# Kernel tuning notes

Hardware: AMD Instinct MI355X
Metric: run time of the kernel (lower is better)

## Reference

```python
import jax, jax.numpy as jnp
import numpy as np
from jax import lax

PRE_NMS_TOPN = 6000
POST_NMS_TOPN = 300
NMS_IOU = 0.7
VARIANCES = np.array([0.1, 0.1, 0.2, 0.2], dtype=np.float32)


def setup_inputs() -> dict:
    key = jax.random.key(0)
    k1, k2, k3, k4 = jax.random.split(key, 4)
    B, FH, FW, K = 32, 128, 128, 9
    A = FH * FW * K  # 147456 total anchors
    rpn_bbox_deltas = jax.random.normal(k1, (B, A, 4), dtype=jnp.float32) * 0.1
    rpn_labels = jax.random.normal(k2, (B, FH, FW, K), dtype=jnp.float32)
    # Anchors in [y1, x1, y2, x2] with y1<y2, x1<x2 on a ~1024px image.
    ctr = jax.random.uniform(k3, (A, 2), dtype=jnp.float32) * 1024.0
    wh = jax.random.uniform(k4, (A, 2), dtype=jnp.float32) * 224.0 + 32.0
    anchors = jnp.concatenate([ctr - 0.5 * wh, ctr + 0.5 * wh], axis=-1)
    return {"rpn_bbox_deltas": rpn_bbox_deltas, "rpn_labels": rpn_labels, "anchors": anchors}


def get_bboxes_from_deltas(anchors, deltas):
    # anchors: [A, 4] (y1,x1,y2,x2); deltas: [B, A, 4] (dy,dx,dh,dw)
    anc_w = anchors[..., 3] - anchors[..., 1]
    anc_h = anchors[..., 2] - anchors[..., 0]
    anc_cx = anchors[..., 1] + 0.5 * anc_w
    anc_cy = anchors[..., 0] + 0.5 * anc_h
    bb_w = jnp.exp(deltas[..., 3]) * anc_w
    bb_h = jnp.exp(deltas[..., 2]) * anc_h
    bb_cx = deltas[..., 1] * anc_w + anc_cx
    bb_cy = deltas[..., 0] * anc_h + anc_cy
    y1 = bb_cy - 0.5 * bb_h
    x1 = bb_cx - 0.5 * bb_w
    y2 = bb_h + y1
    x2 = bb_w + x1
    return jnp.stack([y1, x1, y2, x2], axis=-1)


def nms_per_image(boxes, scores, iou_threshold, num_keep):
    # boxes: [N, 4] sorted by descending score; scores: [N]
    y1, x1, y2, x2 = boxes[:, 0], boxes[:, 1], boxes[:, 2], boxes[:, 3]
    areas = (y2 - y1) * (x2 - x1)

    def step(scores_rem, _):
        idx = jnp.argmax(scores_rem)
        valid = jnp.isfinite(scores_rem[idx])
        b = boxes[idx]
        iy1 = jnp.maximum(b[0], y1)
        ix1 = jnp.maximum(b[1], x1)
        iy2 = jnp.minimum(b[2], y2)
        ix2 = jnp.minimum(b[3], x2)
        inter = jnp.clip(iy2 - iy1, 0.0) * jnp.clip(ix2 - ix1, 0.0)
        b_area = (b[2] - b[0]) * (b[3] - b[1])
        iou = inter / (areas + b_area - inter + 1e-9)
        # IoU(box, itself) == 1 > threshold, so the picked box is also suppressed.
        new_scores = jnp.where(iou > iou_threshold, -jnp.inf, scores_rem)
        return new_scores, (idx, valid)

    _, (keep_idx, valid) = lax.scan(step, scores, None, length=num_keep)
    vf = valid.astype(boxes.dtype)
    keep_boxes = boxes[keep_idx] * vf[:, None]  # zero-pad invalid slots
    keep_scores = scores[keep_idx] * vf
    return keep_boxes, keep_scores


def reference(rpn_bbox_deltas, rpn_labels, anchors):
    A = anchors.shape[0]
    B = rpn_bbox_deltas.shape[0]
    deltas = rpn_bbox_deltas.reshape(B, A, 4) * jnp.asarray(VARIANCES)
    labels = jax.nn.softmax(rpn_labels, axis=-1).reshape(B, A)
    rpn_bboxes = get_bboxes_from_deltas(anchors, deltas)  # [B, A, 4]
    # top-k pre-NMS filter (lax.top_k output is already sorted descending)
    pre_scores, pre_idx = lax.top_k(labels, PRE_NMS_TOPN)  # [B, P]
    pre_boxes = jnp.take_along_axis(rpn_bboxes, pre_idx[..., None], axis=1)  # [B, P, 4]
    nms_fn = lambda b, s: nms_per_image(b, s, NMS_IOU, POST_NMS_TOPN)
    roi_bboxes, roi_scores = jax.vmap(nms_fn)(pre_boxes, pre_scores)
    return roi_bboxes, roi_scores
```

## Files before the change

### kernel.cpp

```cpp
#include <hip/hip_runtime.h>
#include <cstdint>
#include <cstddef>

#pragma clang fp contract(off)

#define KCLS 9
#define PRE_N 6000
#define POST_N 300
#define NMS_IOU_T 0.7f
#define HIST_BLOCK 256
#define CHUNKS_PER_IMG 32
#define NMS_BLOCK 512
#define PICK_BLOCK 256
#define NSEG 8
#define SEG_CAP 2048
#define RANK_LDS 8192

#define SUPP(pb, pa, mbx, mar, out) \
    bool out; { \
        float iy1_ = fmaxf((pb).x, (mbx).x); \
        float ix1_ = fmaxf((pb).y, (mbx).y); \
        float iy2_ = fminf((pb).z, (mbx).z); \
        float ix2_ = fminf((pb).w, (mbx).w); \
        float ih_ = iy2_ - iy1_; ih_ = ih_ > 0.f ? ih_ : 0.f; \
        float iw_ = ix2_ - ix1_; iw_ = iw_ > 0.f ? iw_ : 0.f; \
        float inter_ = ih_ * iw_; \
        float den_ = (mar) + (pa) - inter_ + 1e-9f; \
        float hi_ = 0.7000007f * den_; \
        float lo_ = 0.6999993f * den_; \
        out = inter_ > hi_; \
        if (inter_ >= lo_ && inter_ <= hi_) out = (inter_ / den_) > NMS_IOU_T; \
    }

__global__ void __launch_bounds__(256)
softmax_hist_kernel(const float* __restrict__ labels,
                    float* __restrict__ scores,
                    unsigned int* __restrict__ ghist,
                    int gpi) {
    __shared__ float buf[256 * KCLS];
    __shared__ unsigned int h[2048];
    const int tid = threadIdx.x;
    for (int i = tid; i < 2048; i += 256) h[i] = 0u;

    const size_t gbase = (size_t)blockIdx.x * (256 * KCLS);
    const float4* lin4 = (const float4*)(labels + gbase);
    float4* b4 = (float4*)buf;
    for (int i = tid; i < 576; i += 256) b4[i] = lin4[i];
    __syncthreads();

    float v[KCLS];
    float m = -1e30f;
    #pragma unroll
    for (int k = 0; k < KCLS; ++k) { v[k] = buf[tid * KCLS + k]; m = fmaxf(m, v[k]); }
    float e[KCLS];
    float s = 0.f;
    #pragma unroll
    for (int k = 0; k < KCLS; ++k) { e[k] = expf(v[k] - m); s += e[k]; }
    #pragma unroll
    for (int k = 0; k < KCLS; ++k) {
        float r = e[k] / s;
        buf[tid * KCLS + k] = r;
        atomicAdd(&h[(__float_as_uint(r) >> 21) & 2047u], 1u);
    }
    __syncthreads();

    float4* o4 = (float4*)(scores + gbase);
    for (int i = tid; i < 576; i += 256) o4[i] = b4[i];

    const int img0 = (blockIdx.x * 256) / gpi;
    unsigned int* gh = ghist + (size_t)img0 * 2048;
    for (int i = tid; i < 2048; i += 256) {
        unsigned int c = h[i];
        if (c) atomicAdd(&gh[i], c);
    }
}

__global__ void hist_kernel(const float* __restrict__ scores,
                            unsigned int* __restrict__ ghist,
                            const unsigned int* __restrict__ state,
                            int A, int shift, int bins, unsigned int pmask) {
    __shared__ unsigned int h[2048];
    const int img = blockIdx.y;
    const int chunk = blockIdx.x;
    const int tid = threadIdx.x;
    for (int i = tid; i < bins; i += HIST_BLOCK) h[i] = 0u;
    __syncthreads();
    unsigned int prefix = state[img * 2 + 0] & pmask;
    const int per = A / CHUNKS_PER_IMG;
    const float* sc = scores + (size_t)img * A + (size_t)chunk * per;
    for (int i = tid; i < per; i += HIST_BLOCK) {
        unsigned int v = __float_as_uint(sc[i]);
        if ((v & pmask) == prefix)
            atomicAdd(&h[(v >> shift) & (unsigned)(bins - 1)], 1u);
    }
    __syncthreads();
    unsigned int* gh = ghist + (size_t)img * 2048;
    for (int i = tid; i < bins; i += HIST_BLOCK) {
        unsigned int c = h[i];
        if (c) atomicAdd(&gh[i], c);
    }
}

__global__ void __launch_bounds__(PICK_BLOCK)
pick_kernel(const unsigned int* __restrict__ ghist,
            unsigned int* __restrict__ state,
            int shift, int bins, int first_pass) {
    const int img = blockIdx.x;
    const int t = threadIdx.x;
    const unsigned int* gh = ghist + (size_t)img * 2048;
    __shared__ unsigned int cnt[2048];
    __shared__ unsigned int ssum[PICK_BLOCK];
    const int per = bins / PICK_BLOCK;
    unsigned int my = 0;
    for (int i = 0; i < per; ++i) {
        unsigned int c = gh[t * per + i];
        cnt[t * per + i] = c;
        my += c;
    }
    ssum[t] = my;
    __syncthreads();
    for (int d = 1; d < PICK_BLOCK; d <<= 1) {
        unsigned int v = (t + d < PICK_BLOCK) ? ssum[t + d] : 0u;
        __syncthreads();
        ssum[t] += v;
        __syncthreads();
    }
    unsigned int prefix = first_pass ? 0u : state[img * 2 + 0];
    unsigned int krem = first_pass ? (unsigned)PRE_N : state[img * 2 + 1];
    unsigned int above = ssum[t] - my;
    if (above < krem && ssum[t] >= krem) {
        unsigned int cum = above;
        for (int b = per - 1; b >= 0; --b) {
            unsigned int c = cnt[t * per + b];
            if (cum + c >= krem) {
                state[img * 2 + 0] = prefix | ((unsigned int)(t * per + b) << shift);
                state[img * 2 + 1] = krem - cum;
                break;
            }
            cum += c;
        }
    }
}

#define CE(a, b, u) { if ((v[a] > v[b]) == (u)) { unsigned long long t_ = v[a]; v[a] = v[b]; v[b] = t_; } }
#define REG3(u) { CE(0,4,u) CE(1,5,u) CE(2,6,u) CE(3,7,u) \
                  CE(0,2,u) CE(1,3,u) CE(4,6,u) CE(5,7,u) \
                  CE(0,1,u) CE(2,3,u) CE(4,5,u) CE(6,7,u) }

__global__ void __launch_bounds__(512)
compact_sort_kernel(const float* __restrict__ scores,
                    const unsigned int* __restrict__ state,
                    unsigned long long* __restrict__ pool,
                    unsigned int* __restrict__ counts,
                    int A) {
    __shared__ unsigned long long lin[SEG_CAP];
    __shared__ unsigned int plo[2][SEG_CAP];
    __shared__ unsigned int phi[2][SEG_CAP];
    __shared__ unsigned int cnt;
    const int img = blockIdx.y;
    const int seg = blockIdx.x;
    const int tid = threadIdx.x;
    const int lane = tid & 63;
    const int w = tid >> 6;
    const float* sc = scores + (size_t)img * A;
    const unsigned int T = state[img * 2 + 0];

    if (tid == 0) cnt = 0u;
    for (int i = tid; i < SEG_CAP; i += 512) lin[i] = ~0ull;
    __syncthreads();

    const int ngr = A >> 6;
    const int nj = ngr / NSEG;
    for (int j = w; j < nj; j += 8) {
        int g = seg + j * NSEG;
        int i = (g << 6) + lane;
        unsigned int sv = __float_as_uint(sc[i]);
        bool push = (sv >= T);
        unsigned long long bal = __ballot(push ? 1 : 0);
        if (push) {
            int leader = __ffsll(bal) - 1;
            int rank = __popcll(bal & ((1ull << lane) - 1ull));
            unsigned int base = 0;
            if (lane == leader) base = atomicAdd(&cnt, (unsigned int)__popcll(bal));
            base = (unsigned int)__shfl((int)base, leader);
            unsigned int pos = base + (unsigned int)rank;
            if (pos < SEG_CAP)
                lin[pos] = (((unsigned long long)(~sv)) << 32) | (unsigned long long)(unsigned int)i;
        }
    }
    __syncthreads();

    int n = (int)cnt; if (n > SEG_CAP) n = SEG_CAP;
    int P2 = 512; while (P2 < n) P2 <<= 1;
    const int NT = P2 >> 3;
    const int t = tid;
    const bool act = (t < NT);

    unsigned long long v[8];
    if (act) {
        #pragma unroll
        for (int e = 0; e < 8; ++e) v[e] = lin[(t << 3) + e];
        CE(0,1,true) CE(2,3,false) CE(4,5,true) CE(6,7,false)
        CE(0,2,true) CE(1,3,true) CE(4,6,false) CE(5,7,false)
        CE(0,1,true) CE(2,3,true) CE(4,5,false) CE(6,7,false)
        bool u8 = ((t & 1) == 0);
        REG3(u8)
    }
    int b = 0;
    for (int k = 16; k <= P2; k <<= 1) {
        const bool up = (((t << 3) & k) == 0);
        for (int j = k >> 1; j >= 8; j >>= 1) {
            const int c = j >> 3;
            if (act) {
                #pragma unroll
                for (int e = 0; e < 8; ++e) {
                    int idx = e * NT + t;
                    plo[b][idx] = (unsigned int)v[e];
                    phi[b][idx] = (unsigned int)(v[e] >> 32);
                }
            }
            __syncthreads();
            if (act) {
                const int q = t ^ c;
                const bool keep_min = (up == ((t & c) == 0));
                #pragma unroll
                for (int e = 0; e < 8; ++e) {
                    int idx = e * NT + q;
                    unsigned long long wv = ((unsigned long long)phi[b][idx] << 32)
                                          | (unsigned long long)plo[b][idx];
                    bool less = v[e] < wv;
                    v[e] = (less == keep_min) ? v[e] : wv;
                }
            }
            b ^= 1;
        }
        if (act) { REG3(up) }
    }

    unsigned long long* gp = pool + ((size_t)img * NSEG + seg) * SEG_CAP;
    if (act) {
        #pragma unroll
        for (int e = 0; e < 8; ++e) {
            int r = (t << 3) + e;
            if (r < n) gp[r] = v[e];
        }
    }
    if (tid == 0) counts[img * NSEG + seg] = (unsigned int)n;
}

__global__ void __launch_bounds__(256)
rank_decode_kernel(const unsigned long long* __restrict__ pool,
                   const unsigned int* __restrict__ counts,
                   const float* __restrict__ deltas,
                   const float* __restrict__ anchors,
                   float* __restrict__ pre_boxes,
                   float* __restrict__ pre_scores,
                   int A) {
    __shared__ unsigned long long arr[RANK_LDS];
    const int img = blockIdx.y;
    const int seg = blockIdx.x;
    const int tid = threadIdx.x;

    int c[NSEG], off[NSEG + 1];
    const unsigned long long* gp[NSEG];
    off[0] = 0;
    #pragma unroll
    for (int s = 0; s < NSEG; ++s) {
        int cs = (int)counts[img * NSEG + s];
        if (cs > SEG_CAP) cs = SEG_CAP;
        c[s] = cs;
        off[s + 1] = off[s] + cs;
        gp[s] = pool + ((size_t)img * NSEG + s) * SEG_CAP;
    }
    const int total = off[NSEG];
    const bool inlds = (total <= RANK_LDS);
    if (inlds) {
        #pragma unroll
        for (int s = 0; s < NSEG; ++s)
            for (int i = tid; i < c[s]; i += 256) arr[off[s] + i] = gp[s][i];
    }
    __syncthreads();

    const int m = c[seg];
    for (int i = tid; i < m; i += 256) {
        unsigned long long key = inlds ? arr[off[seg] + i] : gp[seg][i];
        int pos = i;
        #pragma unroll
        for (int s = 0; s < NSEG; ++s) {
            if (s == seg) continue;
            const unsigned long long* base = inlds ? (arr + off[s]) : gp[s];
            int lo = 0, hi = c[s];
            while (lo < hi) {
                int mid = (lo + hi) >> 1;
                if (base[mid] < key) lo = mid + 1; else hi = mid;
            }
            pos += lo;
        }
        if (pos < PRE_N) {
            unsigned int bidx = (unsigned int)(key & 0xFFFFFFFFull);
            unsigned int sbits = ~((unsigned int)(key >> 32));
            float score = __uint_as_float(sbits);
            float a0 = anchors[(size_t)bidx * 4 + 0];
            float a1 = anchors[(size_t)bidx * 4 + 1];
            float a2 = anchors[(size_t)bidx * 4 + 2];
            float a3 = anchors[(size_t)bidx * 4 + 3];
            const float* dd = deltas + ((size_t)img * A + bidx) * 4;
            float d0 = dd[0] * 0.1f;
            float d1 = dd[1] * 0.1f;
            float d2 = dd[2] * 0.2f;
            float d3 = dd[3] * 0.2f;
            float anc_w = a3 - a1;
            float anc_h = a2 - a0;
            float anc_cx = a1 + 0.5f * anc_w;
            float anc_cy = a0 + 0.5f * anc_h;
            float bb_w = expf(d3) * anc_w;
            float bb_h = expf(d2) * anc_h;
            float bb_cx = d1 * anc_w + anc_cx;
            float bb_cy = d0 * anc_h + anc_cy;
            float y1 = bb_cy - 0.5f * bb_h;
            float x1 = bb_cx - 0.5f * bb_w;
            float y2 = bb_h + y1;
            float x2 = bb_w + x1;
            float* ob = pre_boxes + ((size_t)img * PRE_N + pos) * 4;
            ob[0] = y1; ob[1] = x1; ob[2] = y2; ob[3] = x2;
            pre_scores[(size_t)img * PRE_N + pos] = score;
        }
    }
}

__global__ void __launch_bounds__(NMS_BLOCK)
nms_kernel(const float* __restrict__ pre_boxes,
           const float* __restrict__ pre_scores,
           float* __restrict__ out_boxes,
           float* __restrict__ out_scores) {
    const int img = blockIdx.x;
    const int tid = threadIdx.x;
    const int lane = tid & 63;
    const int grp = tid >> 6;
    const float4* bb4 = (const float4*)(pre_boxes + (size_t)img * PRE_N * 4);

    __shared__ float4 kept[POST_N];
    __shared__ float  kept_area[POST_N];
    __shared__ int    kept_idx[POST_N];
    __shared__ float4 chunkbox[2][64];
    __shared__ unsigned long long rows[64];
    __shared__ unsigned long long supball[8];
    __shared__ int kept_cnt;

    const int NCH = (PRE_N + 63) >> 6;

    float4 nb = make_float4(0.f, 0.f, 0.f, 0.f);
    if (tid < 64) {
        chunkbox[0][tid] = bb4[tid];
        nb = bb4[64 + tid];
    }
    if (tid == 0) kept_cnt = 0;
    __syncthreads();

    for (int c = 0; c < NCH; ++c) {
        const int base = c << 6;
        const int cur = c & 1;
        const int K = kept_cnt;
        float4 mb = chunkbox[cur][lane];
        float marea = (mb.z - mb.x) * (mb.w - mb.y);

        bool sup = false;
        for (int k = grp; k < K; k += 8) {
            float4 pb = kept[k];
            float pa = kept_area[k];
            SUPP(pb, pa, mb, marea, s)
            if (s) { sup = true; break; }
        }
        unsigned long long bal = __ballot(sup ? 1 : 0);
        if (lane == 0) supball[grp] = bal;

        #pragma unroll
        for (int u = 0; u < 8; ++u) {
            const int i = (grp << 3) + u;
            float4 pb = chunkbox[cur][i];
            float pa = (pb.z - pb.x) * (pb.w - pb.y);
            SUPP(pb, pa, mb, marea, s)
            unsigned long long rb = __ballot(s ? 1 : 0);
            if (lane == 0) rows[i] = rb;
        }

        if (tid < 64) {
            chunkbox[cur ^ 1][tid] = nb;
            int j = base + 128 + tid;
            nb = (j < PRE_N) ? bb4[j] : make_float4(0.f, 0.f, 0.f, 0.f);
        }
        __syncthreads();

        if (grp == 0) {
            const int remn = PRE_N - base;
            unsigned long long ext = (remn >= 64) ? ~0ull : ((1ull << remn) - 1ull);
            unsigned long long sb = supball[0] | supball[1] | supball[2] | supball[3]
                                  | supball[4] | supball[5] | supball[6] | supball[7];
            unsigned long long rem = ext & ~sb;
            unsigned long long myrow = rows[lane];
            int kc = K;
            while (rem && kc < POST_N) {
                const int i = __ffsll(rem) - 1;
                if (lane == i) {
                    kept[kc] = mb;
                    kept_area[kc] = marea;
                    kept_idx[kc] = base + i;
                }
                unsigned long long ri = __shfl(myrow, i);
                rem &= ~(1ull << i);
                rem &= ~ri;
                ++kc;
            }
            if (lane == 0) kept_cnt = kc;
        }
        __syncthreads();
        if (kept_cnt >= POST_N) break;
    }

    const int kc = kept_cnt;
    for (int r = tid; r < kc; r += NMS_BLOCK) {
        float4 bx = kept[r];
        float* ob = out_boxes + ((size_t)img * POST_N + r) * 4;
        ob[0] = bx.x; ob[1] = bx.y; ob[2] = bx.z; ob[3] = bx.w;
        out_scores[(size_t)img * POST_N + r] =
            pre_scores[(size_t)img * PRE_N + kept_idx[r]];
    }
}

extern "C" void kernel_launch(void* const* d_in, const int* in_sizes, int n_in,
                              void* d_out, int out_size, void* d_ws, size_t ws_size,
                              hipStream_t stream) {
    const float* deltas  = (const float*)d_in[0];
    const float* labels  = (const float*)d_in[1];
    const float* anchors = (const float*)d_in[2];
    float* out = (float*)d_out;

    const int A = in_sizes[2] / 4;
    const int B = in_sizes[0] / (A * 4);
    const int ngroups = in_sizes[1] / KCLS;
    const int gpi = ngroups / B;

    float* scores     = (float*)d_ws;
    float* pre_boxes  = scores + (size_t)B * A;
    float* pre_scores = pre_boxes + (size_t)B * PRE_N * 4;
    unsigned int* hist  = (unsigned int*)(pre_scores + (size_t)B * PRE_N);
    unsigned int* state = hist + (size_t)2 * B * 2048;
    unsigned long long* pool = (unsigned long long*)(state + (size_t)B * 2);
    unsigned int* counts = (unsigned int*)(pool + (size_t)B * NSEG * SEG_CAP);

    float* out_boxes  = out;
    float* out_scores = out + (size_t)B * POST_N * 4;

    hipMemsetAsync(d_out, 0, (size_t)out_size * sizeof(float), stream);
    hipMemsetAsync(hist, 0, ((size_t)2 * B * 2048 + 2 * B) * sizeof(unsigned int), stream);

    softmax_hist_kernel<<<ngroups / 256, 256, 0, stream>>>(
        labels, scores, hist + (size_t)0 * B * 2048, gpi);
    pick_kernel<<<B, PICK_BLOCK, 0, stream>>>(hist + (size_t)0 * B * 2048, state, 21, 2048, 1);

    dim3 hgrid(CHUNKS_PER_IMG, B);
    hist_kernel<<<hgrid, HIST_BLOCK, 0, stream>>>(
        scores, hist + (size_t)1 * B * 2048, state, A, 10, 2048, 0xFFE00000u);
    pick_kernel<<<B, PICK_BLOCK, 0, stream>>>(hist + (size_t)1 * B * 2048, state, 10, 2048, 0);

    dim3 sgrid(NSEG, B);
    compact_sort_kernel<<<sgrid, 512, 0, stream>>>(scores, state, pool, counts, A);
    rank_decode_kernel<<<sgrid, 256, 0, stream>>>(pool, counts, deltas, anchors,
                                                  pre_boxes, pre_scores, A);

    nms_kernel<<<B, NMS_BLOCK, 0, stream>>>(pre_boxes, pre_scores, out_boxes, out_scores);
}
```

Measured before the change: 261.9 us.

## Fuse radix-select pick steps into consumer kernels and replicate softmax histogram bins

Removes the two standalone pick kernels by having each consumer block recompute the threshold-bin selection from the global histograms, so each pass needs one fewer launch and no state buffer round trip. The second-level histogram kernel and the compaction kernel each run the prefix scan redundantly per block. Separately, the softmax histogram uses four sub-bins per bucket keyed by thread index to reduce LDS atomic contention, summing them before the global flush. The cost is redundant scan work in every block and four times the LDS histogram footprint.

```diff
diff --git a/kernel.cpp b/kernel.cpp
--- a/kernel.cpp
+++ b/kernel.cpp
@@ -11,7 +11,6 @@
 #define HIST_BLOCK 256
 #define CHUNKS_PER_IMG 32
 #define NMS_BLOCK 512
-#define PICK_BLOCK 256
 #define NSEG 8
 #define SEG_CAP 2048
 #define RANK_LDS 8192
@@ -32,15 +31,59 @@
         if (inter_ >= lo_ && inter_ <= hi_) out = (inter_ / den_) > NMS_IOU_T; \
     }
 
+__device__ __forceinline__ void pick_dev(
+        const unsigned int* __restrict__ gh,
+        int shift, int bins,
+        unsigned int prefix_in, unsigned int krem_in,
+        unsigned int* cnt,
+        unsigned int* ssum,
+        unsigned int* out) {
+    const int t = threadIdx.x;
+    const int per = bins >> 8;
+    unsigned int my = 0;
+    if (t < 256) {
+        for (int i = 0; i < per; ++i) {
+            unsigned int c = gh[t * per + i];
+            cnt[t * per + i] = c;
+            my += c;
+        }
+        ssum[t] = my;
+    }
+    __syncthreads();
+    for (int d = 1; d < 256; d <<= 1) {
+        unsigned int v = 0u;
+        if (t < 256 && t + d < 256) v = ssum[t + d];
+        __syncthreads();
+        if (t < 256) ssum[t] += v;
+        __syncthreads();
+    }
+    if (t < 256) {
+        unsigned int above = ssum[t] - my;
+        if (above < krem_in && ssum[t] >= krem_in) {
+            unsigned int cum = above;
+            for (int b = per - 1; b >= 0; --b) {
+                unsigned int c = cnt[t * per + b];
+                if (cum + c >= krem_in) {
+                    out[0] = prefix_in | ((unsigned int)(t * per + b) << shift);
+                    out[1] = krem_in - cum;
+                    break;
+                }
+                cum += c;
+            }
+        }
+    }
+    __syncthreads();
+}
+
 __global__ void __launch_bounds__(256)
 softmax_hist_kernel(const float* __restrict__ labels,
                     float* __restrict__ scores,
                     unsigned int* __restrict__ ghist,
                     int gpi) {
     __shared__ float buf[256 * KCLS];
-    __shared__ unsigned int h[2048];
+    __shared__ unsigned int h[2048 * 4];
     const int tid = threadIdx.x;
-    for (int i = tid; i < 2048; i += 256) h[i] = 0u;
+    for (int i = tid; i < 2048 * 4; i += 256) h[i] = 0u;
 
     const size_t gbase = (size_t)blockIdx.x * (256 * KCLS);
     const float4* lin4 = (const float4*)(labels + gbase);
@@ -48,6 +91,7 @@
     for (int i = tid; i < 576; i += 256) b4[i] = lin4[i];
     __syncthreads();
 
+    const int sub = tid & 3;
     float v[KCLS];
     float m = -1e30f;
     #pragma unroll
@@ -60,7 +104,7 @@
     for (int k = 0; k < KCLS; ++k) {
         float r = e[k] / s;
         buf[tid * KCLS + k] = r;
-        atomicAdd(&h[(__float_as_uint(r) >> 21) & 2047u], 1u);
+        atomicAdd(&h[(((__float_as_uint(r) >> 21) & 2047u) << 2) | sub], 1u);
     }
     __syncthreads();
 
@@ -70,75 +114,40 @@
     const int img0 = (blockIdx.x * 256) / gpi;
     unsigned int* gh = ghist + (size_t)img0 * 2048;
     for (int i = tid; i < 2048; i += 256) {
-        unsigned int c = h[i];
+        unsigned int c = h[4 * i] + h[4 * i + 1] + h[4 * i + 2] + h[4 * i + 3];
         if (c) atomicAdd(&gh[i], c);
     }
 }
 
-__global__ void hist_kernel(const float* __restrict__ scores,
-                            unsigned int* __restrict__ ghist,
-                            const unsigned int* __restrict__ state,
-                            int A, int shift, int bins, unsigned int pmask) {
+__global__ void __launch_bounds__(HIST_BLOCK)
+hist2_kernel(const float* __restrict__ scores,
+             const unsigned int* __restrict__ ghist1,
+             unsigned int* __restrict__ ghist2,
+             int A) {
     __shared__ unsigned int h[2048];
+    __shared__ unsigned int ssum[256];
+    __shared__ unsigned int pk[2];
     const int img = blockIdx.y;
     const int chunk = blockIdx.x;
     const int tid = threadIdx.x;
-    for (int i = tid; i < bins; i += HIST_BLOCK) h[i] = 0u;
-    __syncthreads();
-    unsigned int prefix = state[img * 2 + 0] & pmask;
+
+    pick_dev(ghist1 + (size_t)img * 2048, 21, 2048, 0u, (unsigned)PRE_N, h, ssum, pk);
+    const unsigned int prefix = pk[0];
+
+    for (int i = tid; i < 2048; i += HIST_BLOCK) h[i] = 0u;
+    __syncthreads();
     const int per = A / CHUNKS_PER_IMG;
     const float* sc = scores + (size_t)img * A + (size_t)chunk * per;
     for (int i = tid; i < per; i += HIST_BLOCK) {
         unsigned int v = __float_as_uint(sc[i]);
-        if ((v & pmask) == prefix)
-            atomicAdd(&h[(v >> shift) & (unsigned)(bins - 1)], 1u);
-    }
-    __syncthreads();
-    unsigned int* gh = ghist + (size_t)img * 2048;
-    for (int i = tid; i < bins; i += HIST_BLOCK) {
+        if ((v & 0xFFE00000u) == prefix)
+            atomicAdd(&h[(v >> 10) & 2047u], 1u);
+    }
+    __syncthreads();
+    unsigned int* gh = ghist2 + (size_t)img * 2048;
+    for (int i = tid; i < 2048; i += HIST_BLOCK) {
         unsigned int c = h[i];
         if (c) atomicAdd(&gh[i], c);
-    }
-}
-
-__global__ void __launch_bounds__(PICK_BLOCK)
-pick_kernel(const unsigned int* __restrict__ ghist,
-            unsigned int* __restrict__ state,
-            int shift, int bins, int first_pass) {
-    const int img = blockIdx.x;
-    const int t = threadIdx.x;
-    const unsigned int* gh = ghist + (size_t)img * 2048;
-    __shared__ unsigned int cnt[2048];
-    __shared__ unsigned int ssum[PICK_BLOCK];
-    const int per = bins / PICK_BLOCK;
-    unsigned int my = 0;
-    for (int i = 0; i < per; ++i) {
-        unsigned int c = gh[t * per + i];
-        cnt[t * per + i] = c;
-        my += c;
-    }
-    ssum[t] = my;
-    __syncthreads();
-    for (int d = 1; d < PICK_BLOCK; d <<= 1) {
-        unsigned int v = (t + d < PICK_BLOCK) ? ssum[t + d] : 0u;
-        __syncthreads();
-        ssum[t] += v;
-        __syncthreads();
-    }
-    unsigned int prefix = first_pass ? 0u : state[img * 2 + 0];
-    unsigned int krem = first_pass ? (unsigned)PRE_N : state[img * 2 + 1];
-    unsigned int above = ssum[t] - my;
-    if (above < krem && ssum[t] >= krem) {
-        unsigned int cum = above;
-        for (int b = per - 1; b >= 0; --b) {
-            unsigned int c = cnt[t * per + b];
-            if (cum + c >= krem) {
-                state[img * 2 + 0] = prefix | ((unsigned int)(t * per + b) << shift);
-                state[img * 2 + 1] = krem - cum;
-                break;
-            }
-            cum += c;
-        }
     }
 }
 
@@ -149,13 +158,16 @@
 
 __global__ void __launch_bounds__(512)
 compact_sort_kernel(const float* __restrict__ scores,
-                    const unsigned int* __restrict__ state,
+                    const unsigned int* __restrict__ ghist1,
+                    const unsigned int* __restrict__ ghist2,
                     unsigned long long* __restrict__ pool,
                     unsigned int* __restrict__ counts,
                     int A) {
     __shared__ unsigned long long lin[SEG_CAP];
     __shared__ unsigned int plo[2][SEG_CAP];
     __shared__ unsigned int phi[2][SEG_CAP];
+    __shared__ unsigned int ssum[256];
+    __shared__ unsigned int pk[2];
     __shared__ unsigned int cnt;
     const int img = blockIdx.y;
     const int seg = blockIdx.x;
@@ -163,7 +175,13 @@
     const int lane = tid & 63;
     const int w = tid >> 6;
     const float* sc = scores + (size_t)img * A;
-    const unsigned int T = state[img * 2 + 0];
+
+    unsigned int* cnt32 = (unsigned int*)lin;
+    pick_dev(ghist1 + (size_t)img * 2048, 21, 2048, 0u, (unsigned)PRE_N, cnt32, ssum, pk);
+    const unsigned int p1 = pk[0];
+    const unsigned int k1 = pk[1];
+    pick_dev(ghist2 + (size_t)img * 2048, 10, 2048, p1, k1, cnt32, ssum, pk);
+    const unsigned int T = pk[0];
 
     if (tid == 0) cnt = 0u;
     for (int i = tid; i < SEG_CAP; i += 512) lin[i] = ~0ull;
@@ -444,27 +462,25 @@
     float* pre_boxes  = scores + (size_t)B * A;
     float* pre_scores = pre_boxes + (size_t)B * PRE_N * 4;
     unsigned int* hist  = (unsigned int*)(pre_scores + (size_t)B * PRE_N);
-    unsigned int* state = hist + (size_t)2 * B * 2048;
-    unsigned long long* pool = (unsigned long long*)(state + (size_t)B * 2);
+    unsigned long long* pool = (unsigned long long*)(hist + (size_t)2 * B * 2048);
     unsigned int* counts = (unsigned int*)(pool + (size_t)B * NSEG * SEG_CAP);
+
+    unsigned int* ghist1 = hist;
+    unsigned int* ghist2 = hist + (size_t)B * 2048;
 
     float* out_boxes  = out;
     float* out_scores = out + (size_t)B * POST_N * 4;
 
     hipMemsetAsync(d_out, 0, (size_t)out_size * sizeof(float), stream);
-    hipMemsetAsync(hist, 0, ((size_t)2 * B * 2048 + 2 * B) * sizeof(unsigned int), stream);
-
-    softmax_hist_kernel<<<ngroups / 256, 256, 0, stream>>>(
-        labels, scores, hist + (size_t)0 * B * 2048, gpi);
-    pick_kernel<<<B, PICK_BLOCK, 0, stream>>>(hist + (size_t)0 * B * 2048, state, 21, 2048, 1);
+    hipMemsetAsync(hist, 0, (size_t)2 * B * 2048 * sizeof(unsigned int), stream);
+
+    softmax_hist_kernel<<<ngroups / 256, 256, 0, stream>>>(labels, scores, ghist1, gpi);
 
     dim3 hgrid(CHUNKS_PER_IMG, B);
-    hist_kernel<<<hgrid, HIST_BLOCK, 0, stream>>>(
-        scores, hist + (size_t)1 * B * 2048, state, A, 10, 2048, 0xFFE00000u);
-    pick_kernel<<<B, PICK_BLOCK, 0, stream>>>(hist + (size_t)1 * B * 2048, state, 10, 2048, 0);
+    hist2_kernel<<<hgrid, HIST_BLOCK, 0, stream>>>(scores, ghist1, ghist2, A);
 
     dim3 sgrid(NSEG, B);
-    compact_sort_kernel<<<sgrid, 512, 0, stream>>>(scores, state, pool, counts, A);
+    compact_sort_kernel<<<sgrid, 512, 0, stream>>>(scores, ghist1, ghist2, pool, counts, A);
     rank_decode_kernel<<<sgrid, 256, 0, stream>>>(pool, counts, deltas, anchors,
                                                   pre_boxes, pre_scores, A);
 
```

Result: no change. 262.9 us (+0.4%).
